# Optimization experiments

Measured on AMD Instinct MI355X. Metric: run time of the kernel, lower is better.

Reference implementation:

```python
import jax, jax.numpy as jnp
import numpy as np

B, N, DIN, DH, DOUT, H = 64, 512, 256, 512, 256, 4


def setup_inputs() -> dict:
    key = jax.random.key(0)
    ks = jax.random.split(key, 11)
    s = 0.02
    return {
        "x": jax.random.normal(ks[0], (B, N, DIN), jnp.float32),
        # block 0 (in=DIN): per-head embed Linear(DIN,DH) and KQ Linear(DIN,2*DH)
        "e_w0": jax.random.normal(ks[1], (H, DIN, DH), jnp.float32) * s,
        "e_b0": jax.random.normal(ks[2], (H, DH), jnp.float32) * s,
        "kq_w0": jax.random.normal(ks[3], (H, DIN, 2 * DH), jnp.float32) * s,
        "kq_b0": jax.random.normal(ks[4], (H, 2 * DH), jnp.float32) * s,
        # block 1 (in=DH)
        "e_w1": jax.random.normal(ks[5], (H, DH, DH), jnp.float32) * s,
        "e_b1": jax.random.normal(ks[6], (H, DH), jnp.float32) * s,
        "kq_w1": jax.random.normal(ks[7], (H, DH, 2 * DH), jnp.float32) * s,
        "kq_b1": jax.random.normal(ks[8], (H, 2 * DH), jnp.float32) * s,
        # output projection Linear(DH, DOUT)
        "proj_w": jax.random.normal(ks[9], (DH, DOUT), jnp.float32) * s,
        "proj_b": jax.random.normal(ks[10], (DOUT,), jnp.float32) * s,
    }


def _multi_attn(x, ew, eb, kqw, kqb):
    # x: [b,n,d]; ew: [h,d,e]; kqw: [h,d,2e]. num_hidden_layers=2 => each MLP is one Linear.
    embs = jnp.einsum('bnd,hde->hbne', x, ew) + eb[:, None, None, :]
    kq = jnp.einsum('bnd,hdf->hbnf', x, kqw) + kqb[:, None, None, :]
    K, Q = jnp.split(kq, 2, axis=-1)  # torch.chunk order: K first, then Q
    A = jax.nn.softmax(jnp.einsum('hbqe,hbke->hbqk', Q, K), axis=-1)  # unscaled
    out = jnp.einsum('hbqk,hbke->hbqe', A, embs)
    return out.mean(axis=0)  # mean over heads


def reference(x, e_w0, e_b0, kq_w0, kq_b0, e_w1, e_b1, kq_w1, kq_b1, proj_w, proj_b):
    h = _multi_attn(x, e_w0, e_b0, kq_w0, kq_b0)
    h = _multi_attn(h, e_w1, e_b1, kq_w1, kq_b1)
    return h @ proj_w + proj_b
```

## Files before the change

kernel.cpp:

```cpp
#include <hip/hip_runtime.h>

typedef _Float16 half8 __attribute__((ext_vector_type(8)));
typedef _Float16 half4 __attribute__((ext_vector_type(4)));
typedef float floatx4 __attribute__((ext_vector_type(4)));

#define B_    64
#define N_    512
#define DIN_  256
#define DH_   512
#define DOUT_ 256
#define H_    4
#define BN_   (B_ * N_)

#define WAIT_VM4_LGKM0() __builtin_amdgcn_s_waitcnt(0x0074)
#define WAIT_VM0_LGKM0() __builtin_amdgcn_s_waitcnt(0x0070)
#define WAIT_VM4()       __builtin_amdgcn_s_waitcnt(0x0F74)
#define WAIT_VM0()       __builtin_amdgcn_s_waitcnt(0x0F70)
#define MEMBAR()         __asm__ __volatile__("" ::: "memory")
#define BAR()            do { MEMBAR(); __builtin_amdgcn_s_barrier(); MEMBAR(); } while (0)

__device__ static inline void async_copy16(const _Float16* g, _Float16* l) {
    __builtin_amdgcn_global_load_lds(
        (const __attribute__((address_space(1))) void*)g,
        (__attribute__((address_space(3))) void*)l, 16, 0, 0);
}

template <bool OUT_F16>
__global__ __launch_bounds__(256)
void gemm_f16(const _Float16* __restrict__ A, long long aS1, long long aS2, int lda, long long aSeg,
              const _Float16* __restrict__ B, long long bS1, long long bS2, int ldb, long long bSeg,
              void* __restrict__ Cv, long long cS1, long long cS2, int ldc,
              int K, const float* __restrict__ bias, int biasMode,
              long long biasS1, long long biasS2, int zShift)
{
    __shared__ __align__(16) _Float16 As[3][128 * 32];
    __shared__ __align__(16) _Float16 Bs[3][128 * 32];

    const int tid  = threadIdx.x;
    const int wave = tid >> 6;
    const int lane = tid & 63;
    const int quad = lane >> 4;
    const int r16  = lane & 15;

    const int z  = blockIdx.z;
    const int z1 = z >> zShift;
    const int z2 = z & ((1 << zShift) - 1);

    const int gx = gridDim.x, gy = gridDim.y;
    const int T = gx * gy;
    int lin = blockIdx.y * gx + blockIdx.x;
    int id2 = (T & 7) ? lin : ((lin & 7) * (T >> 3) + (lin >> 3));
    const int m0 = (id2 / gx) * 128;
    const int n0 = (id2 % gx) * 128;

    const int srow = lane >> 2;
    const int scol = (((lane & 3) ^ ((lane >> 3) & 3))) * 8;

    const _Float16* gaRow = A + z1 * aS1 + z2 * aS2
                              + (long long)(m0 + wave * 32 + srow) * lda + scol;
    const _Float16* gbRow = B + z1 * bS1 + z2 * bS2
                              + (long long)(n0 + wave * 32 + srow) * ldb + scol;

    const int wm = (wave >> 1) * 64;
    const int wn = (wave & 1) * 64;
    const int gl = (quad ^ ((r16 >> 1) & 3)) * 8;

    floatx4 acc[4][4];
#pragma unroll
    for (int i = 0; i < 4; i++)
#pragma unroll
        for (int j = 0; j < 4; j++) acc[i][j] = (floatx4){0.f, 0.f, 0.f, 0.f};

    auto stage = [&](int p, int k0) {
        const _Float16* a = gaRow + (long long)(k0 >> 9) * aSeg + (k0 & 511);
        const _Float16* b = gbRow + (long long)(k0 >> 9) * bSeg + (k0 & 511);
        _Float16* la = &As[p][wave * 1024];
        _Float16* lb = &Bs[p][wave * 1024];
        async_copy16(a,                    la);
        async_copy16(a + (size_t)16 * lda, la + 512);
        async_copy16(b,                    lb);
        async_copy16(b + (size_t)16 * ldb, lb + 512);
    };

    auto compute = [&](int p) {
        half8 af[4], bf[4];
#pragma unroll
        for (int i = 0; i < 4; i++)
            af[i] = *(const half8*)&As[p][(wm + i * 16 + r16) * 32 + gl];
#pragma unroll
        for (int j = 0; j < 4; j++)
            bf[j] = *(const half8*)&Bs[p][(wn + j * 16 + r16) * 32 + gl];
#pragma unroll
        for (int i = 0; i < 4; i++)
#pragma unroll
            for (int j = 0; j < 4; j++)
                acc[i][j] = __builtin_amdgcn_mfma_f32_16x16x32_f16(
                    bf[j], af[i], acc[i][j], 0, 0, 0);
    };

    const int niter = K >> 5;
    stage(0, 0);
    stage(1, 32);
    int pNext = 2;
    int pCur  = 0;
    for (int it = 0; it < niter - 1; ++it) {
        MEMBAR(); WAIT_VM4_LGKM0();
        __builtin_amdgcn_s_barrier();
        MEMBAR();
        if (it + 2 < niter) stage(pNext, (it + 2) << 5);
        compute(pCur);
        MEMBAR();
        pNext = (pNext == 2) ? 0 : pNext + 1;
        pCur  = (pCur  == 2) ? 0 : pCur  + 1;
    }
    MEMBAR(); WAIT_VM0_LGKM0();
    __builtin_amdgcn_s_barrier(); MEMBAR();
    compute(pCur);

    const float* bz = bias + z1 * biasS1 + z2 * biasS2;
    float*    Cf = (float*)Cv    + z1 * cS1 + z2 * cS2;
    _Float16* Ch = (_Float16*)Cv + z1 * cS1 + z2 * cS2;
#pragma unroll
    for (int i = 0; i < 4; i++) {
        const int row = m0 + wm + i * 16 + r16;
#pragma unroll
        for (int j = 0; j < 4; j++) {
            const int col = n0 + wn + j * 16 + quad * 4;
            float v0 = acc[i][j][0], v1 = acc[i][j][1],
                  v2 = acc[i][j][2], v3 = acc[i][j][3];
            if (biasMode == 1) {
                v0 += bz[col]; v1 += bz[col + 1];
                v2 += bz[col + 2]; v3 += bz[col + 3];
            } else if (biasMode == 2) {
                const float bv = bz[row];
                v0 += bv; v1 += bv; v2 += bv; v3 += bv;
            }
            const size_t idx = (size_t)row * ldc + col;
            if (OUT_F16) {
                half4 hv = {(_Float16)v0, (_Float16)v1, (_Float16)v2, (_Float16)v3};
                *(half4*)&Ch[idx] = hv;
            } else {
                float4 fv = {v0, v1, v2, v3};
                *(float4*)&Cf[idx] = fv;
            }
        }
    }
}

template <bool OUT_F16>
__global__ __launch_bounds__(512, 2)
void gemm256(const _Float16* __restrict__ A, long long aS1, long long aS2, int lda, long long aSeg,
             const _Float16* __restrict__ B, long long bS1, long long bS2, int ldb, long long bSeg,
             void* __restrict__ Cv, long long cS1, long long cS2, int ldc,
             int K, const float* __restrict__ bias, int biasMode,
             long long biasS1, long long biasS2, int zShift)
{
    extern __shared__ __align__(16) _Float16 lds[];
    _Float16* AsB = lds;
    _Float16* BsB = lds + 2 * 256 * 64;

    const int tid  = threadIdx.x;
    const int wave = tid >> 6;
    const int lane = tid & 63;
    const int quad = lane >> 4;
    const int r16  = lane & 15;
    const int wr   = wave >> 2;
    const int wc   = wave & 3;

    const int z  = blockIdx.z;
    const int z1 = z >> zShift;
    const int z2 = z & ((1 << zShift) - 1);

    const int gx = gridDim.x, gy = gridDim.y;
    const int T = gx * gy;
    int lin = blockIdx.y * gx + blockIdx.x;
    int id2 = (T & 7) ? lin : ((lin & 7) * (T >> 3) + (lin >> 3));
    const int m0 = (id2 / gx) * 256;
    const int n0 = (id2 % gx) * 256;

    const int sr  = tid >> 3;
    const int swz = ((tid & 7) ^ (sr & 7)) * 8;
    const _Float16* gaA = A + z1 * aS1 + z2 * aS2 + (long long)(m0 + sr) * lda + swz;
    const _Float16* gbB = B + z1 * bS1 + z2 * bS2 + (long long)(n0 + sr) * ldb + swz;

    const int arow = wr * 64 + r16;
    const int brow = wc * 32 + r16;
    const int rsw  = r16 & 7;
    const int gxk0 = (quad ^ rsw) * 8;
    const int gxk1 = ((4 + quad) ^ rsw) * 8;

    floatx4 acc[8][4];
#pragma unroll
    for (int i = 0; i < 8; i++)
#pragma unroll
        for (int j = 0; j < 4; j++) acc[i][j] = (floatx4){0.f, 0.f, 0.f, 0.f};

    half8 af[4][2], bf[2][2];

    auto stageA = [&](int buf, int h, int tt2) {
        const _Float16* s = gaA + (long long)(h * 128) * lda
                          + (long long)(tt2 >> 3) * aSeg + ((tt2 & 7) << 6);
        _Float16* d = AsB + buf * 16384 + h * 8192 + wave * 512;
        async_copy16(s, d);
        async_copy16(s + (long long)64 * lda, d + 4096);
    };
    auto stageB = [&](int buf, int h, int tt2) {
        const _Float16* s = gbB + (long long)(h * 128) * ldb
                          + (long long)(tt2 >> 3) * bSeg + ((tt2 & 7) << 6);
        _Float16* d = BsB + buf * 16384 + h * 8192 + wave * 512;
        async_copy16(s, d);
        async_copy16(s + (long long)64 * ldb, d + 4096);
    };

#define LOAD_AF(RH, BUF) do { \
    const _Float16* ab_ = AsB + (BUF) * 16384 + ((RH) * 128 + arow) * 64; \
    _Pragma("unroll") \
    for (int i5 = 0; i5 < 4; i5++) { \
        af[i5][0] = *(const half8*)(ab_ + i5 * 1024 + gxk0); \
        af[i5][1] = *(const half8*)(ab_ + i5 * 1024 + gxk1); \
    } \
} while (0)

#define LOAD_BF(CH, BUF) do { \
    const _Float16* bb_ = BsB + (BUF) * 16384 + ((CH) * 128 + brow) * 64; \
    _Pragma("unroll") \
    for (int j5 = 0; j5 < 2; j5++) { \
        bf[j5][0] = *(const half8*)(bb_ + j5 * 1024 + gxk0); \
        bf[j5][1] = *(const half8*)(bb_ + j5 * 1024 + gxk1); \
    } \
} while (0)

#define MFMA16(RH, CH) do { \
    _Pragma("unroll") \
    for (int i6 = 0; i6 < 4; i6++) { \
        _Pragma("unroll") \
        for (int j6 = 0; j6 < 2; j6++) { \
            floatx4 c_ = acc[(RH) * 4 + i6][(CH) * 2 + j6]; \
            c_ = __builtin_amdgcn_mfma_f32_16x16x32_f16(bf[j6][0], af[i6][0], c_, 0, 0, 0); \
            c_ = __builtin_amdgcn_mfma_f32_16x16x32_f16(bf[j6][1], af[i6][1], c_, 0, 0, 0); \
            acc[(RH) * 4 + i6][(CH) * 2 + j6] = c_; \
        } \
    } \
} while (0)

    const int nit = K >> 7;

    stageA(0, 0, 0);
    stageB(0, 1, 0);
    stageA(0, 1, 0);
    stageB(0, 0, 0);
    stageA(1, 0, 1);
    stageB(1, 1, 1);
    WAIT_VM4();
    BAR();

    for (int it = 0; it < nit; ++it) {
        const int tt = it * 2;
        const bool full = (it < nit - 1);

        LOAD_AF(0, 0); LOAD_BF(0, 0);
        stageA(1, 1, tt + 1);
        BAR();
        __builtin_amdgcn_s_setprio(1); MFMA16(0, 0); __builtin_amdgcn_s_setprio(0);
        BAR();
        LOAD_BF(1, 0);
        stageB(1, 0, tt + 1);
        BAR();
        __builtin_amdgcn_s_setprio(1); MFMA16(0, 1); __builtin_amdgcn_s_setprio(0);
        BAR();
        LOAD_AF(1, 0);
        if (full) stageA(0, 0, tt + 2);
        BAR();
        __builtin_amdgcn_s_setprio(1); MFMA16(1, 1); __builtin_amdgcn_s_setprio(0);
        BAR();
        LOAD_BF(0, 0);
        if (full) stageB(0, 1, tt + 2);
        BAR();
        __builtin_amdgcn_s_setprio(1); MFMA16(1, 0); __builtin_amdgcn_s_setprio(0);
        if (full) WAIT_VM4(); else WAIT_VM0();
        BAR();
        LOAD_AF(0, 1); LOAD_BF(0, 1);
        if (full) stageA(0, 1, tt + 2);
        BAR();
        __builtin_amdgcn_s_setprio(1); MFMA16(0, 0); __builtin_amdgcn_s_setprio(0);
        BAR();
        LOAD_BF(1, 1);
        if (full) stageB(0, 0, tt + 2);
        BAR();
        __builtin_amdgcn_s_setprio(1); MFMA16(0, 1); __builtin_amdgcn_s_setprio(0);
        BAR();
        LOAD_AF(1, 1);
        if (full) stageA(1, 0, tt + 3);
        BAR();
        __builtin_amdgcn_s_setprio(1); MFMA16(1, 1); __builtin_amdgcn_s_setprio(0);
        BAR();
        LOAD_BF(0, 1);
        if (full) stageB(1, 1, tt + 3);
        BAR();
        __builtin_amdgcn_s_setprio(1); MFMA16(1, 0); __builtin_amdgcn_s_setprio(0);
        if (full) WAIT_VM4();
        BAR();
    }

#undef LOAD_AF
#undef LOAD_BF
#undef MFMA16

    const float* bz = bias + z1 * biasS1 + z2 * biasS2;
    float*    Cf = (float*)Cv    + z1 * cS1 + z2 * cS2;
    _Float16* Ch = (_Float16*)Cv + z1 * cS1 + z2 * cS2;
#pragma unroll
    for (int f = 0; f < 8; f++) {
        const int row = m0 + (f >> 2) * 128 + wr * 64 + (f & 3) * 16 + r16;
#pragma unroll
        for (int j = 0; j < 4; j++) {
            const int col = n0 + (j >> 1) * 128 + wc * 32 + (j & 1) * 16 + quad * 4;
            float v0 = acc[f][j][0], v1 = acc[f][j][1],
                  v2 = acc[f][j][2], v3 = acc[f][j][3];
            if (biasMode == 1) {
                v0 += bz[col]; v1 += bz[col + 1];
                v2 += bz[col + 2]; v3 += bz[col + 3];
            } else if (biasMode == 2) {
                const float bv = bz[row];
                v0 += bv; v1 += bv; v2 += bv; v3 += bv;
            }
            const size_t idx = (size_t)row * ldc + col;
            if (OUT_F16) {
                half4 hv = {(_Float16)v0, (_Float16)v1, (_Float16)v2, (_Float16)v3};
                *(half4*)&Ch[idx] = hv;
            } else {
                float4 fv = {v0, v1, v2, v3};
                *(float4*)&Cf[idx] = fv;
            }
        }
    }
}

__global__ __launch_bounds__(256)
void softmax_f16(_Float16* __restrict__ S)
{
    const int row  = blockIdx.x * 4 + (threadIdx.x >> 6);
    const int lane = threadIdx.x & 63;
    _Float16* s = S + (size_t)row * 512 + lane * 8;
    half8 h = *(const half8*)s;
    float v[8];
    float mx = -1e30f;
#pragma unroll
    for (int j = 0; j < 8; j++) { v[j] = (float)h[j]; mx = fmaxf(mx, v[j]); }
#pragma unroll
    for (int off = 32; off; off >>= 1) mx = fmaxf(mx, __shfl_xor(mx, off));
    float sum = 0.f;
#pragma unroll
    for (int j = 0; j < 8; j++) { v[j] = __expf(v[j] - mx); sum += v[j]; }
#pragma unroll
    for (int off = 32; off; off >>= 1) sum += __shfl_xor(sum, off);
    const float inv = 0.25f / sum;
#pragma unroll
    for (int j = 0; j < 8; j++) h[j] = (_Float16)(v[j] * inv);
    *(half8*)s = h;
}

__global__ __launch_bounds__(256)
void cvt_f32_f16(const float* __restrict__ in, _Float16* __restrict__ out)
{
    const size_t i = ((size_t)blockIdx.x * blockDim.x + threadIdx.x) * 4;
    const float4 f = *(const float4*)(in + i);
    out[i + 0] = (_Float16)f.x;
    out[i + 1] = (_Float16)f.y;
    out[i + 2] = (_Float16)f.z;
    out[i + 3] = (_Float16)f.w;
}

__global__ __launch_bounds__(256)
void transpose_cvt(const float* __restrict__ in, _Float16* __restrict__ out,
                   int R, int C)
{
    __shared__ float tile[32][33];
    const int g  = blockIdx.z;
    const int c0 = blockIdx.x * 32;
    const int r0 = blockIdx.y * 32;
    const float* inp  = in  + (size_t)g * R * C;
    _Float16*    outp = out + (size_t)g * R * C;
#pragma unroll
    for (int i = threadIdx.y; i < 32; i += 8)
        tile[i][threadIdx.x] = inp[(size_t)(r0 + i) * C + c0 + threadIdx.x];
    __syncthreads();
#pragma unroll
    for (int i = threadIdx.y; i < 32; i += 8)
        outp[(size_t)(c0 + i) * R + r0 + threadIdx.x] = (_Float16)tile[threadIdx.x][i];
}

__global__ __launch_bounds__(256)
void wk_bq(const float* __restrict__ kq_w, const float* __restrict__ kq_b,
           float* __restrict__ w, int dinShift)
{
    const int t = blockIdx.x * 256 + threadIdx.x;
    const int h = t >> dinShift;
    const int d = t & ((1 << dinShift) - 1);
    const float* wk = kq_w + ((size_t)(h << dinShift) + d) * (2 * DH_);
    const float* bq = kq_b + (size_t)h * 2 * DH_ + DH_;
    float s = 0.f;
    for (int e = 0; e < DH_; e++) s += wk[e] * bq[e];
    w[t] = s;
}

__global__ __launch_bounds__(256)
void fold_bias(const _Float16* __restrict__ projwT, const float* __restrict__ e_b1,
               float* __restrict__ be1p)
{
    const int t = blockIdx.x * 256 + threadIdx.x;
    const int h = t >> 8;
    const int o = t & 255;
    const _Float16* pw = projwT + (size_t)o * DH_;
    const float*    eb = e_b1 + (size_t)h * DH_;
    float s = 0.f;
    for (int d = 0; d < DH_; d++) s += (float)pw[d] * eb[d];
    be1p[t] = s;
}

__global__ __launch_bounds__(256)
void compute_v(const _Float16* __restrict__ x, const float* __restrict__ w,
               float* __restrict__ V, int Kin)
{
    const int row  = blockIdx.x * 4 + (threadIdx.x >> 6);
    const int lane = threadIdx.x & 63;
    const int b = row >> 9, n = row & 511;
    const _Float16* xr = x + (size_t)row * Kin;
    float s0 = 0.f, s1 = 0.f, s2 = 0.f, s3 = 0.f;
    const int iters = Kin >> 6;
    for (int j = 0; j < iters; j++) {
        const int idx = lane + j * 64;
        const float xv = (float)xr[idx];
        s0 += xv * w[idx];
        s1 += xv * w[Kin + idx];
        s2 += xv * w[2 * Kin + idx];
        s3 += xv * w[3 * Kin + idx];
    }
#pragma unroll
    for (int off = 32; off; off >>= 1) {
        s0 += __shfl_xor(s0, off); s1 += __shfl_xor(s1, off);
        s2 += __shfl_xor(s2, off); s3 += __shfl_xor(s3, off);
    }
    if (lane == 0) {
        float* vb = V + ((size_t)b * H_) * N_ + n;
        vb[0] = s0; vb[N_] = s1; vb[2 * N_] = s2; vb[3 * N_] = s3;
    }
}

extern "C" void kernel_launch(void* const* d_in, const int* in_sizes, int n_in,
                              void* d_out, int out_size, void* d_ws, size_t ws_size,
                              hipStream_t stream)
{
    (void)in_sizes; (void)n_in; (void)out_size;

    static bool attr_set = false;
    if (!attr_set) {
        hipFuncSetAttribute((const void*)gemm256<true>,
                            hipFuncAttributeMaxDynamicSharedMemorySize, 131072);
        hipFuncSetAttribute((const void*)gemm256<false>,
                            hipFuncAttributeMaxDynamicSharedMemorySize, 131072);
        attr_set = true;
    }

    const float* x      = (const float*)d_in[0];
    const float* e_w0   = (const float*)d_in[1];
    const float* e_b0   = (const float*)d_in[2];
    const float* kq_w0  = (const float*)d_in[3];
    const float* kq_b0  = (const float*)d_in[4];
    const float* e_w1   = (const float*)d_in[5];
    const float* e_b1   = (const float*)d_in[6];
    const float* kq_w1  = (const float*)d_in[7];
    const float* kq_b1  = (const float*)d_in[8];
    const float* proj_w = (const float*)d_in[9];
    const float* proj_b = (const float*)d_in[10];
    float* out = (float*)d_out;

    char* ws = (char*)d_ws;
    size_t off = 0;
    auto alloc = [&](size_t bytes) -> char* {
        char* p = ws + off;
        off += (bytes + 255) & ~(size_t)255;
        return p;
    };

    _Float16* x16    = (_Float16*)alloc((size_t)BN_ * DIN_ * 2);
    _Float16* h1_16  = (_Float16*)alloc((size_t)BN_ * DH_ * 2);
    _Float16* kq0_16 = (_Float16*)alloc((size_t)H_ * DIN_ * 2 * DH_ * 2);
    _Float16* kq1_16 = (_Float16*)alloc((size_t)H_ * DH_ * 2 * DH_ * 2);
    _Float16* ew1_16 = (_Float16*)alloc((size_t)H_ * DH_ * DH_ * 2);
    _Float16* ewT0   = (_Float16*)alloc((size_t)H_ * DH_ * DIN_ * 2);
    _Float16* projwT = (_Float16*)alloc((size_t)DOUT_ * DH_ * 2);
    _Float16* Mt0    = (_Float16*)alloc((size_t)H_ * DIN_ * DIN_ * 2);
    _Float16* Mt1    = (_Float16*)alloc((size_t)H_ * DH_ * DH_ * 2);
    _Float16* We1pT  = (_Float16*)alloc((size_t)H_ * DOUT_ * DH_ * 2);
    float*    be1p   = (float*)alloc((size_t)H_ * DOUT_ * 4);
    float*    w0     = (float*)alloc((size_t)H_ * DIN_ * 4);
    float*    w1     = (float*)alloc((size_t)H_ * DH_ * 4);
    float*    Vb     = (float*)alloc((size_t)B_ * H_ * N_ * 4);

    const size_t persist = off;
    auto chunkBytes = [](int ch) {
        return (size_t)ch * N_ * H_ * DH_ * 2
             + (size_t)ch * H_ * N_ * N_ * 2
             + (size_t)ch * H_ * DH_ * N_ * 2;
    };
    int CH = 8;
    if (ws_size >= persist + chunkBytes(32) + (1u << 20)) CH = 32;
    else if (ws_size >= persist + chunkBytes(16) + (1u << 20)) CH = 16;
    const int NCH = B_ / CH;

    _Float16* Tc   = (_Float16*)alloc((size_t)CH * N_ * H_ * DH_ * 2);
    _Float16* Sc   = (_Float16*)alloc((size_t)CH * H_ * N_ * N_ * 2);
    _Float16* embc = (_Float16*)alloc((size_t)CH * H_ * DH_ * N_ * 2);

    auto gemm = [&](bool outF16,
                    const _Float16* A, long long aS1, long long aS2, int lda, long long aSeg,
                    const _Float16* Bp, long long bS1, long long bS2, int ldb, long long bSeg,
                    void* C, long long cS1, long long cS2, int ldc,
                    int M, int Nn, int K, int batches, int zShift,
                    const float* bias, int biasMode, long long biasS1, long long biasS2) {
        const bool big = (M % 256 == 0) && (Nn % 256 == 0) && (K % 128 == 0)
                       && ((long long)(M >> 8) * (Nn >> 8) * batches >= 32);
        if (big) {
            dim3 grid(Nn / 256, M / 256, batches), block(512);
            if (outF16)
                gemm256<true><<<grid, block, 131072, stream>>>(A, aS1, aS2, lda, aSeg,
                    Bp, bS1, bS2, ldb, bSeg, C, cS1, cS2, ldc, K, bias, biasMode, biasS1, biasS2, zShift);
            else
                gemm256<false><<<grid, block, 131072, stream>>>(A, aS1, aS2, lda, aSeg,
                    Bp, bS1, bS2, ldb, bSeg, C, cS1, cS2, ldc, K, bias, biasMode, biasS1, biasS2, zShift);
        } else {
            dim3 grid(Nn / 128, M / 128, batches), block(256);
            if (outF16)
                gemm_f16<true><<<grid, block, 0, stream>>>(A, aS1, aS2, lda, aSeg,
                    Bp, bS1, bS2, ldb, bSeg, C, cS1, cS2, ldc, K, bias, biasMode, biasS1, biasS2, zShift);
            else
                gemm_f16<false><<<grid, block, 0, stream>>>(A, aS1, aS2, lda, aSeg,
                    Bp, bS1, bS2, ldb, bSeg, C, cS1, cS2, ldc, K, bias, biasMode, biasS1, biasS2, zShift);
        }
    };

    cvt_f32_f16<<<BN_ * DIN_ / 1024, 256, 0, stream>>>(x, x16);
    cvt_f32_f16<<<H_ * DIN_ * 2 * DH_ / 1024, 256, 0, stream>>>(kq_w0, kq0_16);
    cvt_f32_f16<<<H_ * DH_ * 2 * DH_ / 1024, 256, 0, stream>>>(kq_w1, kq1_16);
    cvt_f32_f16<<<H_ * DH_ * DH_ / 1024, 256, 0, stream>>>(e_w1, ew1_16);
    transpose_cvt<<<dim3(DH_ / 32, DIN_ / 32, H_), dim3(32, 8), 0, stream>>>(e_w0, ewT0, DIN_, DH_);
    transpose_cvt<<<dim3(DOUT_ / 32, DH_ / 32, 1), dim3(32, 8), 0, stream>>>(proj_w, projwT, DH_, DOUT_);

    gemm(true, kq0_16, 0, (long long)DIN_ * 2 * DH_, 2 * DH_, 512,
         kq0_16 + DH_, 0, (long long)DIN_ * 2 * DH_, 2 * DH_, 512,
         Mt0, 0, (long long)DIN_ * DIN_, DIN_,
         DIN_, DIN_, DH_, H_, 2, nullptr, 0, 0, 0);
    gemm(true, kq1_16, 0, (long long)DH_ * 2 * DH_, 2 * DH_, 512,
         kq1_16 + DH_, 0, (long long)DH_ * 2 * DH_, 2 * DH_, 512,
         Mt1, 0, (long long)DH_ * DH_, DH_,
         DH_, DH_, DH_, H_, 2, nullptr, 0, 0, 0);
    gemm(true, projwT, 0, 0, DH_, 512,
         ew1_16, 0, (long long)DH_ * DH_, DH_, 512,
         We1pT, 0, (long long)DOUT_ * DH_, DH_,
         DOUT_, DH_, DH_, H_, 2, nullptr, 0, 0, 0);
    fold_bias<<<H_ * DOUT_ / 256, 256, 0, stream>>>(projwT, e_b1, be1p);
    wk_bq<<<H_ * DIN_ / 256, 256, 0, stream>>>(kq_w0, kq_b0, w0, 8);
    wk_bq<<<H_ * DH_ / 256, 256, 0, stream>>>(kq_w1, kq_b1, w1, 9);

    const long long SB = (long long)N_ * N_;

    for (int blk = 0; blk < 2; blk++) {
        const _Float16* xin = blk ? h1_16 : x16;
        const int       Kin = blk ? DH_ : DIN_;
        const _Float16* Mt  = blk ? Mt1 : Mt0;
        const float*    wv  = blk ? w1 : w0;

        compute_v<<<BN_ / 4, 256, 0, stream>>>(xin, wv, Vb, Kin);

        for (int c = 0; c < NCH; c++) {
            const _Float16* xc = xin + (size_t)c * CH * N_ * Kin;

            gemm(true, xc, 0, 0, Kin, 512,
                 Mt, 0, 0, Kin, 512,
                 Tc, 0, 0, H_ * Kin,
                 CH * N_, H_ * Kin, Kin, 1, 0, nullptr, 0, 0, 0);
            gemm(true, Tc, (long long)N_ * H_ * Kin, Kin, H_ * Kin, 512,
                 xc, (long long)N_ * Kin, 0, Kin, 512,
                 Sc, (long long)H_ * SB, SB, N_,
                 N_, N_, Kin, CH * H_, 2,
                 Vb + (size_t)c * CH * H_ * N_, 1, (long long)H_ * N_, N_);
            softmax_f16<<<CH * H_ * N_ / 4, 256, 0, stream>>>(Sc);

            if (blk == 0) {
                gemm(true, ewT0, 0, 0, Kin, 512,
                     xc, (long long)N_ * Kin, 0, Kin, 512,
                     embc, (long long)H_ * DH_ * N_, 0, N_,
                     H_ * DH_, N_, Kin, CH, 0, e_b0, 2, 0, 0);
                gemm(true, Sc, (long long)H_ * SB, 0, N_, SB,
                     embc, (long long)H_ * DH_ * N_, 0, N_, (long long)DH_ * N_,
                     h1_16 + (size_t)c * CH * N_ * DH_, (long long)N_ * DH_, 0, DH_,
                     N_, DH_, H_ * N_, CH, 0, nullptr, 0, 0, 0);
            } else {
                gemm(true, We1pT, 0, 0, DH_, 512,
                     xc, (long long)N_ * DH_, 0, DH_, 512,
                     embc, (long long)H_ * DOUT_ * N_, 0, N_,
                     H_ * DOUT_, N_, DH_, CH, 0, be1p, 2, 0, 0);
                gemm(false, Sc, (long long)H_ * SB, 0, N_, SB,
                     embc, (long long)H_ * DOUT_ * N_, 0, N_, (long long)DOUT_ * N_,
                     out + (size_t)c * CH * N_ * DOUT_, (long long)N_ * DOUT_, 0, DOUT_,
                     N_, DOUT_, H_ * N_, CH, 0, proj_b, 1, 0, 0);
            }
        }
    }
}
```

Measured before the change: 1.045 ms.

## Double-buffer B fragments in GEMM and batch final attention GEMMs over full batch

The GEMM main loop keeps two sets of B-operand register fragments, so the B tile for column half 0 is reused across the row-half pass and two LDS reloads per half-iteration are dropped. The host side gains a mode where, when the workspace is large enough, full-batch score and embedding buffers are allocated. The attention-times-embedding GEMM then runs once over all 64 batches instead of once per chunk. This cuts launch count and improves grid fill, but it needs much more workspace and more VGPRs for the extra fragments.

```diff
diff --git a/kernel.cpp b/kernel.cpp
--- a/kernel.cpp
+++ b/kernel.cpp
@@ -195,7 +195,7 @@
 #pragma unroll
         for (int j = 0; j < 4; j++) acc[i][j] = (floatx4){0.f, 0.f, 0.f, 0.f};
 
-    half8 af[4][2], bf[2][2];
+    half8 af[4][2], bf0s[2][2], bf1s[2][2];
 
     auto stageA = [&](int buf, int h, int tt2) {
         const _Float16* s = gaA + (long long)(h * 128) * lda
@@ -221,23 +221,23 @@
     } \
 } while (0)
 
-#define LOAD_BF(CH, BUF) do { \
+#define LOAD_BF(DST, CH, BUF) do { \
     const _Float16* bb_ = BsB + (BUF) * 16384 + ((CH) * 128 + brow) * 64; \
     _Pragma("unroll") \
     for (int j5 = 0; j5 < 2; j5++) { \
-        bf[j5][0] = *(const half8*)(bb_ + j5 * 1024 + gxk0); \
-        bf[j5][1] = *(const half8*)(bb_ + j5 * 1024 + gxk1); \
+        DST[j5][0] = *(const half8*)(bb_ + j5 * 1024 + gxk0); \
+        DST[j5][1] = *(const half8*)(bb_ + j5 * 1024 + gxk1); \
     } \
 } while (0)
 
-#define MFMA16(RH, CH) do { \
+#define MFMA16(RH, CH, BFS) do { \
     _Pragma("unroll") \
     for (int i6 = 0; i6 < 4; i6++) { \
         _Pragma("unroll") \
         for (int j6 = 0; j6 < 2; j6++) { \
             floatx4 c_ = acc[(RH) * 4 + i6][(CH) * 2 + j6]; \
-            c_ = __builtin_amdgcn_mfma_f32_16x16x32_f16(bf[j6][0], af[i6][0], c_, 0, 0, 0); \
-            c_ = __builtin_amdgcn_mfma_f32_16x16x32_f16(bf[j6][1], af[i6][1], c_, 0, 0, 0); \
+            c_ = __builtin_amdgcn_mfma_f32_16x16x32_f16(BFS[j6][0], af[i6][0], c_, 0, 0, 0); \
+            c_ = __builtin_amdgcn_mfma_f32_16x16x32_f16(BFS[j6][1], af[i6][1], c_, 0, 0, 0); \
             acc[(RH) * 4 + i6][(CH) * 2 + j6] = c_; \
         } \
     } \
@@ -258,46 +258,44 @@
         const int tt = it * 2;
         const bool full = (it < nit - 1);
 
-        LOAD_AF(0, 0); LOAD_BF(0, 0);
+        LOAD_AF(0, 0); LOAD_BF(bf0s, 0, 0);
         stageA(1, 1, tt + 1);
         BAR();
-        __builtin_amdgcn_s_setprio(1); MFMA16(0, 0); __builtin_amdgcn_s_setprio(0);
-        BAR();
-        LOAD_BF(1, 0);
+        __builtin_amdgcn_s_setprio(1); MFMA16(0, 0, bf0s); __builtin_amdgcn_s_setprio(0);
+        BAR();
+        LOAD_BF(bf1s, 1, 0);
         stageB(1, 0, tt + 1);
         BAR();
-        __builtin_amdgcn_s_setprio(1); MFMA16(0, 1); __builtin_amdgcn_s_setprio(0);
+        __builtin_amdgcn_s_setprio(1); MFMA16(0, 1, bf1s); __builtin_amdgcn_s_setprio(0);
         BAR();
         LOAD_AF(1, 0);
         if (full) stageA(0, 0, tt + 2);
         BAR();
-        __builtin_amdgcn_s_setprio(1); MFMA16(1, 1); __builtin_amdgcn_s_setprio(0);
-        BAR();
-        LOAD_BF(0, 0);
+        __builtin_amdgcn_s_setprio(1); MFMA16(1, 1, bf1s); __builtin_amdgcn_s_setprio(0);
+        BAR();
         if (full) stageB(0, 1, tt + 2);
         BAR();
-        __builtin_amdgcn_s_setprio(1); MFMA16(1, 0); __builtin_amdgcn_s_setprio(0);
+        __builtin_amdgcn_s_setprio(1); MFMA16(1, 0, bf0s); __builtin_amdgcn_s_setprio(0);
         if (full) WAIT_VM4(); else WAIT_VM0();
         BAR();
-        LOAD_AF(0, 1); LOAD_BF(0, 1);
+        LOAD_AF(0, 1); LOAD_BF(bf0s, 0, 1);
         if (full) stageA(0, 1, tt + 2);
         BAR();
-        __builtin_amdgcn_s_setprio(1); MFMA16(0, 0); __builtin_amdgcn_s_setprio(0);
-        BAR();
-        LOAD_BF(1, 1);
+        __builtin_amdgcn_s_setprio(1); MFMA16(0, 0, bf0s); __builtin_amdgcn_s_setprio(0);
+        BAR();
+        LOAD_BF(bf1s, 1, 1);
         if (full) stageB(0, 0, tt + 2);
         BAR();
-        __builtin_amdgcn_s_setprio(1); MFMA16(0, 1); __builtin_amdgcn_s_setprio(0);
+        __builtin_amdgcn_s_setprio(1); MFMA16(0, 1, bf1s); __builtin_amdgcn_s_setprio(0);
         BAR();
         LOAD_AF(1, 1);
         if (full) stageA(1, 0, tt + 3);
         BAR();
-        __builtin_amdgcn_s_setprio(1); MFMA16(1, 1); __builtin_amdgcn_s_setprio(0);
-        BAR();
-        LOAD_BF(0, 1);
+        __builtin_amdgcn_s_setprio(1); MFMA16(1, 1, bf1s); __builtin_amdgcn_s_setprio(0);
+        BAR();
         if (full) stageB(1, 1, tt + 3);
         BAR();
-        __builtin_amdgcn_s_setprio(1); MFMA16(1, 0); __builtin_amdgcn_s_setprio(0);
+        __builtin_amdgcn_s_setprio(1); MFMA16(1, 0, bf0s); __builtin_amdgcn_s_setprio(0);
         if (full) WAIT_VM4();
         BAR();
     }
@@ -499,19 +497,36 @@
     float*    Vb     = (float*)alloc((size_t)B_ * H_ * N_ * 4);
 
     const size_t persist = off;
-    auto chunkBytes = [](int ch) {
-        return (size_t)ch * N_ * H_ * DH_ * 2
+    const size_t SLACK    = 1u << 20;
+    const size_t SC_FULL  = (size_t)B_ * H_ * N_ * N_ * 2;
+    const size_t EMB_FULL = (size_t)B_ * H_ * DH_ * N_ * 2;
+    auto tcBytes = [](int ch) { return (size_t)ch * N_ * H_ * DH_ * 2; };
+    auto chunkBytes = [&](int ch) {
+        return tcBytes(ch)
              + (size_t)ch * H_ * N_ * N_ * 2
              + (size_t)ch * H_ * DH_ * N_ * 2;
     };
-    int CH = 8;
-    if (ws_size >= persist + chunkBytes(32) + (1u << 20)) CH = 32;
-    else if (ws_size >= persist + chunkBytes(16) + (1u << 20)) CH = 16;
+
+    int mode, CH;
+    if (ws_size >= persist + tcBytes(64) + SC_FULL + EMB_FULL + SLACK)      { mode = 2; CH = 64; }
+    else if (ws_size >= persist + tcBytes(32) + SC_FULL + EMB_FULL + SLACK) { mode = 1; CH = 32; }
+    else {
+        mode = 0; CH = 8;
+        if (ws_size >= persist + chunkBytes(32) + SLACK) CH = 32;
+        else if (ws_size >= persist + chunkBytes(16) + SLACK) CH = 16;
+    }
     const int NCH = B_ / CH;
 
-    _Float16* Tc   = (_Float16*)alloc((size_t)CH * N_ * H_ * DH_ * 2);
-    _Float16* Sc   = (_Float16*)alloc((size_t)CH * H_ * N_ * N_ * 2);
-    _Float16* embc = (_Float16*)alloc((size_t)CH * H_ * DH_ * N_ * 2);
+    _Float16 *Tc, *Sc, *embc;
+    if (mode >= 1) {
+        Tc   = (_Float16*)alloc(tcBytes(CH));
+        Sc   = (_Float16*)alloc(SC_FULL);
+        embc = (_Float16*)alloc(EMB_FULL);
+    } else {
+        Tc   = (_Float16*)alloc(tcBytes(CH));
+        Sc   = (_Float16*)alloc((size_t)CH * H_ * N_ * N_ * 2);
+        embc = (_Float16*)alloc((size_t)CH * H_ * DH_ * N_ * 2);
+    }
 
     auto gemm = [&](bool outF16,
                     const _Float16* A, long long aS1, long long aS2, int lda, long long aSeg,
@@ -568,6 +583,7 @@
     for (int blk = 0; blk < 2; blk++) {
         const _Float16* xin = blk ? h1_16 : x16;
         const int       Kin = blk ? DH_ : DIN_;
+        const int       E   = blk ? DOUT_ : DH_;
         const _Float16* Mt  = blk ? Mt1 : Mt0;
         const float*    wv  = blk ? w1 : w0;
 
@@ -575,6 +591,8 @@
 
         for (int c = 0; c < NCH; c++) {
             const _Float16* xc = xin + (size_t)c * CH * N_ * Kin;
+            _Float16* Scp  = Sc   + (mode >= 1 ? (size_t)c * CH * H_ * SB : 0);
+            _Float16* embp = embc + (mode >= 1 ? (size_t)c * CH * H_ * E * N_ : 0);
 
             gemm(true, xc, 0, 0, Kin, 512,
                  Mt, 0, 0, Kin, 512,
@@ -582,29 +600,47 @@
                  CH * N_, H_ * Kin, Kin, 1, 0, nullptr, 0, 0, 0);
             gemm(true, Tc, (long long)N_ * H_ * Kin, Kin, H_ * Kin, 512,
                  xc, (long long)N_ * Kin, 0, Kin, 512,
-                 Sc, (long long)H_ * SB, SB, N_,
+                 Scp, (long long)H_ * SB, SB, N_,
                  N_, N_, Kin, CH * H_, 2,
                  Vb + (size_t)c * CH * H_ * N_, 1, (long long)H_ * N_, N_);
-            softmax_f16<<<CH * H_ * N_ / 4, 256, 0, stream>>>(Sc);
+            softmax_f16<<<CH * H_ * N_ / 4, 256, 0, stream>>>(Scp);
 
             if (blk == 0) {
                 gemm(true, ewT0, 0, 0, Kin, 512,
                      xc, (long long)N_ * Kin, 0, Kin, 512,
-                     embc, (long long)H_ * DH_ * N_, 0, N_,
+                     embp, (long long)H_ * DH_ * N_, 0, N_,
                      H_ * DH_, N_, Kin, CH, 0, e_b0, 2, 0, 0);
-                gemm(true, Sc, (long long)H_ * SB, 0, N_, SB,
-                     embc, (long long)H_ * DH_ * N_, 0, N_, (long long)DH_ * N_,
-                     h1_16 + (size_t)c * CH * N_ * DH_, (long long)N_ * DH_, 0, DH_,
-                     N_, DH_, H_ * N_, CH, 0, nullptr, 0, 0, 0);
+                if (mode == 0) {
+                    gemm(true, Scp, (long long)H_ * SB, 0, N_, SB,
+                         embp, (long long)H_ * DH_ * N_, 0, N_, (long long)DH_ * N_,
+                         h1_16 + (size_t)c * CH * N_ * DH_, (long long)N_ * DH_, 0, DH_,
+                         N_, DH_, H_ * N_, CH, 0, nullptr, 0, 0, 0);
+                }
             } else {
                 gemm(true, We1pT, 0, 0, DH_, 512,
                      xc, (long long)N_ * DH_, 0, DH_, 512,
-                     embc, (long long)H_ * DOUT_ * N_, 0, N_,
+                     embp, (long long)H_ * DOUT_ * N_, 0, N_,
                      H_ * DOUT_, N_, DH_, CH, 0, be1p, 2, 0, 0);
+                if (mode == 0) {
+                    gemm(false, Scp, (long long)H_ * SB, 0, N_, SB,
+                         embp, (long long)H_ * DOUT_ * N_, 0, N_, (long long)DOUT_ * N_,
+                         out + (size_t)c * CH * N_ * DOUT_, (long long)N_ * DOUT_, 0, DOUT_,
+                         N_, DOUT_, H_ * N_, CH, 0, proj_b, 1, 0, 0);
+                }
+            }
+        }
+
+        if (mode >= 1) {
+            if (blk == 0) {
+                gemm(true, Sc, (long long)H_ * SB, 0, N_, SB,
+                     embc, (long long)H_ * DH_ * N_, 0, N_, (long long)DH_ * N_,
+                     h1_16, (long long)N_ * DH_, 0, DH_,
+                     N_, DH_, H_ * N_, B_, 0, nullptr, 0, 0, 0);
+            } else {
                 gemm(false, Sc, (long long)H_ * SB, 0, N_, SB,
                      embc, (long long)H_ * DOUT_ * N_, 0, N_, (long long)DOUT_ * N_,
-                     out + (size_t)c * CH * N_ * DOUT_, (long long)N_ * DOUT_, 0, DOUT_,
-                     N_, DOUT_, H_ * N_, CH, 0, proj_b, 1, 0, 0);
+                     out, (long long)N_ * DOUT_, 0, DOUT_,
+                     N_, DOUT_, H_ * N_, B_, 0, proj_b, 1, 0, 0);
             }
         }
     }
```

New measurement: 1.062 ms. About the same (+1.7%).
